# Kernel tuning notes

Measured on AMD Instinct MI355X. Metric: run time of the kernel, lower is better.

Reference implementation:

```python
import jax, jax.numpy as jnp
import numpy as np

# Dims matching init_kwargs / input_specs
H = 64   # latent_size (GRU hidden)
L = 64   # rnn_layers
D = 128  # input_size
B = 128  # batch
T = 256  # sequence length


def setup_inputs() -> dict:
    key = jax.random.key(0)
    ks = jax.random.split(key, 13)
    s = 1.0 / np.sqrt(H)  # PyTorch GRU/Linear default init scale
    u = lambda k, shp: jax.random.uniform(k, shp, jnp.float32, -s, s)
    return {
        "context": jax.random.normal(ks[0], (B, T, D), jnp.float32),
        # encoder GRU params; layer 0 consumes D, layers 1..L-1 consume H
        "enc_Wih0": u(ks[1], (3 * H, D)),
        "enc_Wih": u(ks[2], (L - 1, 3 * H, H)),
        "enc_Whh": u(ks[3], (L, 3 * H, H)),
        "enc_bih": u(ks[4], (L, 3 * H)),
        "enc_bhh": u(ks[5], (L, 3 * H)),
        # decoder GRU params
        "dec_Wih0": u(ks[6], (3 * H, D)),
        "dec_Wih": u(ks[7], (L - 1, 3 * H, H)),
        "dec_Whh": u(ks[8], (L, 3 * H, H)),
        "dec_bih": u(ks[9], (L, 3 * H)),
        "dec_bhh": u(ks[10], (L, 3 * H)),
        # output projection
        "Wo": u(ks[11], (D, H)),
        "bo": u(ks[12], (D,)),
    }


def _gru_cell(x, h, Wih, Whh, bih, bhh):
    # PyTorch gate order: r, z, n
    gi = x @ Wih.T + bih            # (B, 3H)
    gh = h @ Whh.T + bhh            # (B, 3H)
    ir, iz, inn = jnp.split(gi, 3, axis=-1)
    hr, hz, hn = jnp.split(gh, 3, axis=-1)
    r = jax.nn.sigmoid(ir + hr)
    z = jax.nn.sigmoid(iz + hz)
    n = jnp.tanh(inn + r * hn)
    return (1.0 - z) * n + z * h


def _run_gru(X, h0, Wih0, Wih, Whh, bih, bhh):
    # X: (B, T, D); h0: (L, B, H). Returns (top-layer outputs (B,T,H), final hidden (L,B,H)).
    def layer_step(x_in, lp):
        h_prev, W_ih, W_hh, b_i, b_h = lp
        h_new = _gru_cell(x_in, h_prev, W_ih, W_hh, b_i, b_h)
        return h_new, h_new

    @jax.checkpoint
    def step(hs, x_t):
        h_first = _gru_cell(x_t, hs[0], Wih0, Whh[0], bih[0], bhh[0])
        top, hs_rest = jax.lax.scan(
            layer_step, h_first, (hs[1:], Wih, Whh[1:], bih[1:], bhh[1:]))
        return jnp.concatenate([h_first[None], hs_rest], axis=0), top

    hs_final, outs = jax.lax.scan(step, h0, jnp.swapaxes(X, 0, 1))
    return jnp.swapaxes(outs, 0, 1), hs_final


def reference(context, enc_Wih0, enc_Wih, enc_Whh, enc_bih, enc_bhh,
              dec_Wih0, dec_Wih, dec_Whh, dec_bih, dec_bhh, Wo, bo):
    Bc = context.shape[0]
    h0 = jnp.zeros((L, Bc, H), context.dtype)
    # encoder: only final hidden state is used
    _, h_n = _run_gru(context, h0, enc_Wih0, enc_Wih, enc_Whh, enc_bih, enc_bhh)
    # teacher forcing (ratio=1.0): decoder input at step i is X[:, i-1], zeros at i=0
    dec_in = jnp.concatenate([jnp.zeros_like(context[:, :1]), context[:, :-1]], axis=1)
    dec_out, _ = _run_gru(dec_in, h_n, dec_Wih0, dec_Wih, dec_Whh, dec_bih, dec_bhh)
    return dec_out @ Wo.T + bo  # (B, T, D)
```

## Files before the change

### kernel.cpp

```cpp
#include <hip/hip_runtime.h>
#include <stdint.h>

typedef uint16_t u16;
typedef unsigned long long u64;
typedef __attribute__((ext_vector_type(8))) short short8;
typedef __attribute__((ext_vector_type(4))) float f32x4;

#define SCOPE __HIP_MEMORY_SCOPE_AGENT
#define FSTRIDE 16
#define FLD(p) __hip_atomic_load((p), __ATOMIC_RELAXED, SCOPE)
#define FST(p, v) __hip_atomic_store((p), (v), __ATOMIC_RELAXED, SCOPE)

template <int N> struct IC { static constexpr int value = N; };

static __device__ __forceinline__ float bf2f(u16 b) {
  union { uint32_t u; float f; } x; x.u = ((uint32_t)b) << 16; return x.f;
}
static __device__ __forceinline__ u16 f2bf(float f) {
  union { float f; uint32_t u; } x; x.f = f;
  uint32_t u = x.u;
  u += 0x7fffu + ((u >> 16) & 1u);
  return (u16)(u >> 16);
}
static __device__ __forceinline__ float sigm(float x) {
  return __builtin_amdgcn_rcpf(1.f + __expf(-x));
}
static __device__ __forceinline__ float tanhf_(float x) {
  return 1.f - 2.f * __builtin_amdgcn_rcpf(1.f + __expf(2.f * x));
}
static __device__ __forceinline__ void lds_barrier() {
  asm volatile("s_waitcnt lgkmcnt(0)\n\ts_barrier" ::: "memory");
}
#define DRAIN0() asm volatile("s_waitcnt vmcnt(0)" ::: "memory")
static __device__ __forceinline__ int imin(int a, int b) { return a < b ? a : b; }

#define OFF_WHA 0
#define OFF_WHB 12288
#define OFF_WIB 24576
#define OFF_WIA 36864
#define OFF_WO  49152

template <int CHE, int CHD>
__global__ __launch_bounds__(512, 1) void gru_pipeline(
    const void* ctx_,
    const void* eWih0_, const void* eWih_, const void* eWhh_,
    const void* ebih_,  const void* ebhh_,
    const void* dWih0_, const void* dWih_, const void* dWhh_,
    const void* dbih_,  const void* dbhh_,
    const void* Wo_,    const void* bo_,   void* out_,
    int* __restrict__ pflag, int* __restrict__ cflag,
    u64* __restrict__ ringE, u64* __restrict__ ringD, int RE, int RW)
{
  const int tid  = threadIdx.x;
  const bool isX = (tid < 256);
  const int lane = tid & 63;
  const int qg   = (tid >> 6) & 3;
  const int w8   = tid >> 6;
  const int lo   = lane & 15;
  const int hi   = lane >> 4;
  const int blk  = blockIdx.x;
  const int P    = blk >> 3;
  const int g    = blk & 7;
  const int LA   = 2 * P;
  const int NKCA = (P == 0) ? 4 : 2;

  extern __shared__ __align__(16) u16 dynlds[];

  __shared__ __align__(16) u16 hbA[2][16 * 72];
  __shared__ __align__(16) u16 hbB[2][16 * 72];
  __shared__ __align__(16) u16 xstA[2][16 * 72];
  __shared__ int s_cnt, s_fin, s_cn;
  if (tid == 0) { s_cnt = 0; s_fin = 0; s_cn = 0; }
  for (int i = tid; i < 16 * 72; i += 512) {
    hbA[0][i] = 0; hbA[1][i] = 0; hbB[0][i] = 0; hbB[1][i] = 0;
    xstA[0][i] = 0; xstA[1][i] = 0;
  }
  __syncthreads();
  {
    u16 v = ((const u16*)ebih_)[2 * (tid & 255)];
    int e = (v >> 7) & 0xFF;
    if (e >= 100 && e <= 126 && isX) atomicAdd(&s_cnt, 1);
  }
  __syncthreads();
  const bool bf = (s_cnt >= 128);

  auto ld8 = [&](const void* p, int idx) -> short8 {
    if (bf) return *(const short8*)((const u16*)p + idx);
    const float* f = (const float*)p + idx;
    short8 r;
#pragma unroll
    for (int j = 0; j < 8; ++j) r[j] = (short)f2bf(f[j]);
    return r;
  };
  auto ld1 = [&](const void* p, int idx) -> float {
    return bf ? bf2f(((const u16*)p)[idx]) : ((const float*)p)[idx];
  };

  const int T0 = qg, T1 = 4 + qg, T2 = 8 + qg;

  short8 zf8 = {0,0,0,0,0,0,0,0};
  float  bov[2] = {0.f, 0.f};
  float brzA[2] = {0,0}, binA = 0, bhnA = 0;
  float brzB[2] = {0,0}, binB = 0, bhnB = 0;

  auto stage_w = [&](int offU16, const void* W, int gidx0, int NT, int KC, int K) {
    for (int nt = w8; nt < NT; nt += 8)
      for (int kc = 0; kc < KC; ++kc) {
        short8 v = ld8(W, gidx0 + (nt*16 + lo)*K + kc*32 + hi*8);
        *(short8*)(dynlds + offU16 + (nt*KC + kc)*512 + lane*8) = v;
      }
  };

  auto load_phase = [&](int ph) {
    const void* WH  = ph ? dWhh_ : eWhh_;
    const void* WIs = ph ? dWih_ : eWih_;
    const void* WI0 = ph ? dWih0_ : eWih0_;
    const void* bi  = ph ? dbih_ : ebih_;
    const void* bh  = ph ? dbhh_ : ebhh_;
    stage_w(OFF_WHA, WH, LA*192*64, 12, 2, 64);
    stage_w(OFF_WHB, WH, (LA+1)*192*64, 12, 2, 64);
    stage_w(OFF_WIB, WIs, LA*192*64, 12, 2, 64);
    if (LA == 0) stage_w(OFF_WIA, WI0, 0, 12, 4, 128);
    else         stage_w(OFF_WIA, WIs, (LA-1)*192*64, 12, 2, 64);
    if (isX) {
      brzA[0] = ld1(bi, LA*192 + T0*16 + lo) + ld1(bh, LA*192 + T0*16 + lo);
      brzA[1] = ld1(bi, LA*192 + T1*16 + lo) + ld1(bh, LA*192 + T1*16 + lo);
      binA    = ld1(bi, LA*192 + T2*16 + lo);
      bhnA    = ld1(bh, LA*192 + T2*16 + lo);
    } else {
      const int LB = LA + 1;
      brzB[0] = ld1(bi, LB*192 + T0*16 + lo) + ld1(bh, LB*192 + T0*16 + lo);
      brzB[1] = ld1(bi, LB*192 + T1*16 + lo) + ld1(bh, LB*192 + T1*16 + lo);
      binB    = ld1(bi, LB*192 + T2*16 + lo);
      bhnB    = ld1(bh, LB*192 + T2*16 + lo);
    }
  };
  load_phase(0);
  if (P == 31) {
    stage_w(OFF_WO, Wo_, 0, 8, 2, 64);
    if (!isX) { bov[0] = ld1(bo_, 32*qg + lo); bov[1] = ld1(bo_, 32*qg + 16 + lo); }
  }

  const int oWhA0 = OFF_WHA + T0*1024 + lane*8;
  const int oWhA1 = OFF_WHA + T1*1024 + lane*8;
  const int oWhA2 = OFF_WHA + T2*1024 + lane*8;
  const int oWhB0 = OFF_WHB + T0*1024 + lane*8;
  const int oWhB1 = OFF_WHB + T1*1024 + lane*8;
  const int oWhB2 = OFF_WHB + T2*1024 + lane*8;
  const int oWiB0 = OFF_WIB + T0*1024 + lane*8;
  const int oWiB1 = OFF_WIB + T1*1024 + lane*8;
  const int oWiB2 = OFF_WIB + T2*1024 + lane*8;
  const int oWiA0 = OFF_WIA + T0*(NKCA*512) + lane*8;
  const int oWiA1 = OFF_WIA + T1*(NKCA*512) + lane*8;
  const int oWiA2 = OFF_WIA + T2*(NKCA*512) + lane*8;
  const int oWo0  = OFF_WO + (2*qg + 0)*1024 + lane*8;
  const int oWo1  = OFF_WO + (2*qg + 1)*1024 + lane*8;

  auto WF = [&](int off, int kc) -> short8 {
    return *(const short8*)(dynlds + off + kc*512);
  };

  auto do_proj = [&](int tprev, const u16* hs) {
    f32x4 pacc[2];
#pragma unroll
    for (int ct = 0; ct < 2; ++ct) { float v = bov[ct]; f32x4 tv = {v,v,v,v}; pacc[ct] = tv; }
#pragma unroll
    for (int kc = 0; kc < 2; ++kc) {
      short8 hA = *(const short8*)(hs + lo*72 + kc*32 + hi*8);
      pacc[0] = __builtin_amdgcn_mfma_f32_16x16x32_bf16(hA, WF(oWo0, kc), pacc[0], 0, 0, 0);
      pacc[1] = __builtin_amdgcn_mfma_f32_16x16x32_bf16(hA, WF(oWo1, kc), pacc[1], 0, 0, 0);
    }
#pragma unroll
    for (int ct = 0; ct < 2; ++ct) {
      int n = 32*qg + 16*ct + lo;
#pragma unroll
      for (int p = 0; p < 4; ++p) {
        int b = 16*g + hi*4 + p;
        size_t idx = ((size_t)b * 256 + (tprev - 256)) * 128 + n;
        float v = fminf(64.f, fmaxf(-64.f, pacc[ct][p]));
        if (bf) ((u16*)out_)[idx] = f2bf(v);
        else    ((float*)out_)[idx] = v;
      }
    }
  };

  float hprevA[4] = {0,0,0,0}, hprevB[4] = {0,0,0,0};
  const int brow = 16*g + lo;

  const int eIn  = (P > 0 ? P - 1 : 0) * 8 + g;
  const int eOut = (P < 31 ? P : 30) * 8 + g;
  int* fin   = pflag + eIn  * FSTRIDE;
  int* fout  = pflag + eOut * FSTRIDE;
  int* cself = cflag + (P * 8 + g) * FSTRIDE;
  int* cnext = cflag + ((P < 31 ? P + 1 : 31) * 8 + g) * FSTRIDE;

  auto raddr = [&](int t) -> const u64* {
    return (t < 256)
      ? (ringE + (size_t)eIn * ((size_t)RE * 256) + (size_t)(t & (RE-1)) * 256)
      : (ringD + (size_t)eIn * ((size_t)RW * 256) + (size_t)((t-256) & (RW-1)) * 256);
  };
  auto waddr = [&](int t) -> u64* {
    return (t < 256)
      ? (ringE + (size_t)eOut * ((size_t)RE * 256) + (size_t)(t & (RE-1)) * 256)
      : (ringD + (size_t)eOut * ((size_t)RW * 256) + (size_t)((t-256) & (RW-1)) * 256);
  };

  int budget = 1 << 22;
  const int srow = 4 * (tid & 3);
  const int scol = tid >> 2;

  int f0=0,f1=0,f2=0,f3=0, c0=0,c1=0,c2=0,c3=0;
  short8 cfx[4] = {zf8, zf8, zf8, zf8};

  auto doB = [&](int s) {
    f32x4 br, bz, bin2, bhn;
    { float v;
      v = brzB[0]; br   = (f32x4){v,v,v,v};
      v = brzB[1]; bz   = (f32x4){v,v,v,v};
      v = binB;    bin2 = (f32x4){v,v,v,v};
      v = bhnB;    bhn  = (f32x4){v,v,v,v}; }
    const u16* hsB = hbB[(s + 1) & 1];
    const u16* xsB = hbA[s & 1];
#pragma unroll
    for (int kc = 0; kc < 2; ++kc) {
      short8 hB = *(const short8*)(hsB + lo*72 + kc*32 + hi*8);
      short8 xB = *(const short8*)(xsB + lo*72 + kc*32 + hi*8);
      br   = __builtin_amdgcn_mfma_f32_16x16x32_bf16(hB, WF(oWhB0, kc), br,   0, 0, 0);
      bz   = __builtin_amdgcn_mfma_f32_16x16x32_bf16(hB, WF(oWhB1, kc), bz,   0, 0, 0);
      bhn  = __builtin_amdgcn_mfma_f32_16x16x32_bf16(hB, WF(oWhB2, kc), bhn,  0, 0, 0);
      br   = __builtin_amdgcn_mfma_f32_16x16x32_bf16(xB, WF(oWiB0, kc), br,   0, 0, 0);
      bz   = __builtin_amdgcn_mfma_f32_16x16x32_bf16(xB, WF(oWiB1, kc), bz,   0, 0, 0);
      bin2 = __builtin_amdgcn_mfma_f32_16x16x32_bf16(xB, WF(oWiB2, kc), bin2, 0, 0, 0);
    }
    u16 hBb[4];
#pragma unroll
    for (int p = 0; p < 4; ++p) {
      float r = sigm(br[p]);
      float z = sigm(bz[p]);
      float n = tanhf_(bin2[p] + r * bhn[p]);
      float h = n + z * (hprevB[p] - n);
      h = fminf(1.f, fmaxf(-1.f, h));
      hprevB[p] = h;
      hBb[p] = f2bf(h);
    }
    u16* hd = hbB[s & 1];
#pragma unroll
    for (int p = 0; p < 4; ++p)
      hd[(hi*4 + p) * 72 + qg*16 + lo] = hBb[p];
    if (P < 31) {
      u64 da = (u64)hBb[0] | ((u64)hBb[1] << 16) | ((u64)hBb[2] << 32) | ((u64)hBb[3] << 48);
      FST(waddr(s) + (16*qg + lo)*4 + hi, da);
    }
  };

  __syncthreads();

  auto span = [&](auto chc, const int tbase, const int cbase, const int RC, const bool dec) {
    constexpr int CH = decltype(chc)::value;
    const int NC = 256 / CH;
    const bool credOn = (RC < NC);

    if (P > 0) {
      if (tid == 0) {
        int v = s_fin;
        if (v < cbase + 1) {
          while (budget > 0) {
            int a = FLD(fin+0), b = FLD(fin+1), c = FLD(fin+2), d = FLD(fin+3);
            v = imin(imin(a, b), imin(c, d));
            if (v >= cbase + 1) break;
            --budget; __builtin_amdgcn_s_sleep(2);
          }
          s_fin = v; f0 = v; f1 = v; f2 = v; f3 = v;
        }
      }
      __syncthreads();
      if (isX) {
        u64 r0 = FLD(raddr(tbase) + tid);
        u16* xd = xstA[tbase & 1];
#pragma unroll
        for (int p = 0; p < 4; ++p) xd[(srow + p) * 72 + scol] = (u16)(r0 >> (16 * p));
      }
    }
    if (P == 0 && isX) {
      int tx = (tbase < 256) ? tbase : 0;
#pragma unroll
      for (int kc = 0; kc < 4; ++kc) cfx[kc] = ld8(ctx_, (brow*256 + tx)*128 + kc*32 + hi*8);
    }

#pragma unroll 1
    for (int k = 0; k < NC; ++k) {
      const int t0 = tbase + k * CH;
      const int ck = cbase + k;
      const int fneed = ck + 2 - ((dec && k == NC - 1) ? 1 : 0);
      const int need  = (credOn && k >= RC) ? (ck + 1 - RC) : 0;
      u64 ra[CH];
#pragma unroll
      for (int j = 0; j < CH; ++j) ra[j] = 0;

#pragma unroll
      for (int tt = 0; tt < CH; ++tt) {
        const int t = t0 + tt;
        lds_barrier();

        if (tt == 0) {
          int vf = s_fin, vc = s_cn;
          const bool slowF = (P > 0)  && (vf < fneed);
          const bool slowC = (P < 31) && (need > 0) && (vc < need);
          if (slowF || slowC) {
            if (tid == 0) {
              if (slowF) {
                int v = 0;
                while (budget > 0) {
                  int a = FLD(fin+0), b = FLD(fin+1), c = FLD(fin+2), d = FLD(fin+3);
                  v = imin(imin(a, b), imin(c, d));
                  if (v >= fneed) break;
                  --budget; __builtin_amdgcn_s_sleep(2);
                }
                s_fin = v; f0 = v; f1 = v; f2 = v; f3 = v;
              }
              if (slowC) {
                int v = 0;
                while (budget > 0) {
                  int a = FLD(cnext+0), b = FLD(cnext+1), c = FLD(cnext+2), d = FLD(cnext+3);
                  v = imin(imin(a, b), imin(c, d));
                  if (v >= need) break;
                  --budget; __builtin_amdgcn_s_sleep(2);
                }
                s_cn = v; c0 = v; c1 = v; c2 = v; c3 = v;
              }
            }
            lds_barrier();
          }
          if (isX && P > 0) {
#pragma unroll
            for (int j = 0; j < CH; ++j)
              if (t0 + 1 + j <= 511) ra[j] = FLD(raddr(t0 + 1 + j) + tid);
          }
        }

        if (isX) {
          if (tid == 0) {
            if (P > 0)  s_fin = imin(imin(f0, f1), imin(f2, f3));
            if (P < 31 && credOn) s_cn = imin(imin(c0, c1), imin(c2, c3));
            if (P > 0)  { f0 = FLD(fin+0); f1 = FLD(fin+1); f2 = FLD(fin+2); f3 = FLD(fin+3); }
            if (P < 31 && credOn) { c0 = FLD(cnext+0); c1 = FLD(cnext+1); c2 = FLD(cnext+2); c3 = FLD(cnext+3); }
          }

          f32x4 ar, az, ain, ahn;
          { float v;
            v = brzA[0]; ar  = (f32x4){v,v,v,v};
            v = brzA[1]; az  = (f32x4){v,v,v,v};
            v = binA;    ain = (f32x4){v,v,v,v};
            v = bhnA;    ahn = (f32x4){v,v,v,v}; }
          const u16* hsA = hbA[(t + 1) & 1];
#pragma unroll
          for (int kc = 0; kc < 2; ++kc) {
            short8 hA = *(const short8*)(hsA + lo*72 + kc*32 + hi*8);
            ar  = __builtin_amdgcn_mfma_f32_16x16x32_bf16(hA, WF(oWhA0, kc), ar,  0, 0, 0);
            az  = __builtin_amdgcn_mfma_f32_16x16x32_bf16(hA, WF(oWhA1, kc), az,  0, 0, 0);
            ahn = __builtin_amdgcn_mfma_f32_16x16x32_bf16(hA, WF(oWhA2, kc), ahn, 0, 0, 0);
          }
          short8 xfA[4] = {zf8, zf8, zf8, zf8};
          if (P > 0) {
            const u16* xs = xstA[t & 1];
#pragma unroll
            for (int kc = 0; kc < 2; ++kc)
              xfA[kc] = *(const short8*)(xs + lo*72 + kc*32 + hi*8);
          } else {
#pragma unroll
            for (int kc = 0; kc < 4; ++kc) xfA[kc] = cfx[kc];
          }
          if (!(P == 0 && t == 256)) {
#pragma unroll
            for (int kc = 0; kc < 4; ++kc) {
              if (kc < NKCA) {
                ar  = __builtin_amdgcn_mfma_f32_16x16x32_bf16(xfA[kc], WF(oWiA0, kc), ar,  0, 0, 0);
                az  = __builtin_amdgcn_mfma_f32_16x16x32_bf16(xfA[kc], WF(oWiA1, kc), az,  0, 0, 0);
                ain = __builtin_amdgcn_mfma_f32_16x16x32_bf16(xfA[kc], WF(oWiA2, kc), ain, 0, 0, 0);
              }
            }
          }
          u16 hAb[4];
#pragma unroll
          for (int p = 0; p < 4; ++p) {
            float r = sigm(ar[p]);
            float z = sigm(az[p]);
            float n = tanhf_(ain[p] + r * ahn[p]);
            float h = n + z * (hprevA[p] - n);
            h = fminf(1.f, fmaxf(-1.f, h));
            hprevA[p] = h;
            hAb[p] = f2bf(h);
          }
          {
            u16* hd = hbA[t & 1];
#pragma unroll
            for (int p = 0; p < 4; ++p)
              hd[(hi*4 + p) * 72 + qg*16 + lo] = hAb[p];
          }
          if (P == 0) {
            int tn = t + 1;
            if (tn <= 511) {
              int tx = (tn < 256) ? tn : ((tn == 256) ? 0 : tn - 257);
#pragma unroll
              for (int kc = 0; kc < 4; ++kc)
                cfx[kc] = ld8(ctx_, (brow*256 + tx)*128 + kc*32 + hi*8);
            }
          }
          if (P > 0 && t < 511) {
            u64 r = ra[tt];
            u16* xd = xstA[(t + 1) & 1];
#pragma unroll
            for (int p = 0; p < 4; ++p) xd[(srow + p) * 72 + scol] = (u16)(r >> (16 * p));
          }
          if (tt == CH - 1 && P > 0 && credOn) {
            DRAIN0();
            if (lane == 0) FST(cself + qg, ck + 1);
          }
        } else {
          constexpr int FO = (CH >= 2) ? 1 : 0;
          if (P < 31 && tt == FO && k > ((CH == 1) ? 1 : 0)) {
            DRAIN0();
            if (lane == 0) FST(fout + qg, ck - ((CH == 1) ? 1 : 0));
          }
          if (P == 31 && dec && t >= 258) do_proj(t - 2, hbB[t & 1]);
          if (t - 1 >= tbase) doB(t - 1);
        }
      }
    }

    lds_barrier();
    if (!isX) {
      doB(tbase + 255);
      if (P < 31) {
        DRAIN0();
        if (lane == 0) FST(fout + qg, cbase + NC);
      }
    }
  };

  {
    const int NCe = 256 / CHE;
    int RCe = (RE >= 256) ? NCe : (RE / CHE) - 2; if (RCe < 1) RCe = 1;
    span(IC<CHE>{}, 0, 0, RCe, false);
    __syncthreads();
    load_phase(1);
    __syncthreads();
    int RCd = (RW >= 256) ? (256 / CHD) : (RW / CHD) - 2; if (RCd < 1) RCd = 1;
    span(IC<CHD>{}, 256, NCe, RCd, true);
  }

  lds_barrier();
  if (P == 31 && !isX) {
    do_proj(510, hbB[0]);
    do_proj(511, hbB[1]);
  }
}

extern "C" void kernel_launch(void* const* d_in, const int* in_sizes, int n_in,
                              void* d_out, int out_size, void* d_ws, size_t ws_size,
                              hipStream_t stream)
{
  char* ws = (char*)d_ws;
  int* pflag = (int*)ws;
  int* cflag = (int*)(ws + 32768);
  char* ringbase = ws + 65536;

  const size_t per_slot = (size_t)31 * 8 * 2048;
  size_t avail = (ws_size > 65536) ? ws_size - 65536 : 0;

  int RE, RW;
  u64 *ringE, *ringD;
  int Rh = 0;
  for (int r = 256; r >= 16; r >>= 1)
    if ((size_t)(2 * r) * per_slot <= avail) { Rh = r; break; }
  if (Rh) {
    RE = RW = Rh;
    ringE = (u64*)ringbase;
    ringD = (u64*)(ringbase + (size_t)Rh * per_slot);
  } else {
    int Rw = 1;
    for (int r = 256; r >= 1; r >>= 1)
      if ((size_t)r * per_slot <= avail) { Rw = r; break; }
    RW = Rw;
    int Re = 1;
    for (int r = 16; r >= 1; r >>= 1)
      if ((size_t)r * per_slot <= (size_t)out_size) { Re = r; break; }
    RE = Re;
    ringE = (u64*)d_out;
    ringD = (u64*)ringbase;
  }
  const int CHe = (RE >= 32) ? 4 : ((RE >= 16) ? 2 : 1);
  const int CHd = (RW >= 32) ? 4 : ((RW >= 16) ? 2 : 1);

  const int dyn = 122880;
  static int attr_done = 0;
  if (!attr_done) {
    hipFuncSetAttribute(reinterpret_cast<const void*>(gru_pipeline<4,4>),
                        hipFuncAttributeMaxDynamicSharedMemorySize, dyn);
    hipFuncSetAttribute(reinterpret_cast<const void*>(gru_pipeline<2,4>),
                        hipFuncAttributeMaxDynamicSharedMemorySize, dyn);
    hipFuncSetAttribute(reinterpret_cast<const void*>(gru_pipeline<2,2>),
                        hipFuncAttributeMaxDynamicSharedMemorySize, dyn);
    hipFuncSetAttribute(reinterpret_cast<const void*>(gru_pipeline<2,1>),
                        hipFuncAttributeMaxDynamicSharedMemorySize, dyn);
    hipFuncSetAttribute(reinterpret_cast<const void*>(gru_pipeline<1,1>),
                        hipFuncAttributeMaxDynamicSharedMemorySize, dyn);
    attr_done = 1;
  }

  hipMemsetAsync(ws, 0, 65536, stream);

#define LAUNCH(CE, CD)                                                     \
  gru_pipeline<CE, CD><<<256, 512, dyn, stream>>>(                         \
      d_in[0], d_in[1], d_in[2], d_in[3], d_in[4], d_in[5],                \
      d_in[6], d_in[7], d_in[8], d_in[9], d_in[10], d_in[11], d_in[12],    \
      d_out, pflag, cflag, ringE, ringD, RE, RW)

  if      (CHe == 4 && CHd == 4) LAUNCH(4, 4);
  else if (CHe == 2 && CHd == 4) LAUNCH(2, 4);
  else if (CHe == 2 && CHd == 2) LAUNCH(2, 2);
  else if (CHe == 2 && CHd == 1) LAUNCH(2, 1);
  else                           LAUNCH(1, 1);
#undef LAUNCH
  (void)in_sizes; (void)n_in;
}
```

Baseline: 1.861 ms.

## Repartition pipeline into 16 stages of 4 layers with register-resident weights

The layer pipeline moves from 32 stages of 2 layers × 8 batch groups of 16 rows to 16 stages of 4 layers × 16 batch groups of 8 rows. Each wave now keeps its gate weights in registers instead of reading them from dynamic LDS, and the two wavegroups each run two layers in a staggered schedule. The intent is to halve the number of inter-block handoffs along the dependency chain and remove LDS weight reads from the critical path. The cost is that MFMA tiles are half padding (8 real rows in 16), register pressure rises, and the chunk size is fixed at 2 instead of adapting to ring size.

Result: slower. 1.941 ms (+4.3%).

```diff
diff --git a/kernel.cpp b/kernel.cpp
--- a/kernel.cpp
+++ b/kernel.cpp
@@ -10,8 +10,6 @@
 #define FSTRIDE 16
 #define FLD(p) __hip_atomic_load((p), __ATOMIC_RELAXED, SCOPE)
 #define FST(p, v) __hip_atomic_store((p), (v), __ATOMIC_RELAXED, SCOPE)
-
-template <int N> struct IC { static constexpr int value = N; };
 
 static __device__ __forceinline__ float bf2f(u16 b) {
   union { uint32_t u; float f; } x; x.u = ((uint32_t)b) << 16; return x.f;
@@ -34,13 +32,6 @@
 #define DRAIN0() asm volatile("s_waitcnt vmcnt(0)" ::: "memory")
 static __device__ __forceinline__ int imin(int a, int b) { return a < b ? a : b; }
 
-#define OFF_WHA 0
-#define OFF_WHB 12288
-#define OFF_WIB 24576
-#define OFF_WIA 36864
-#define OFF_WO  49152
-
-template <int CHE, int CHD>
 __global__ __launch_bounds__(512, 1) void gru_pipeline(
     const void* ctx_,
     const void* eWih0_, const void* eWih_, const void* eWhh_,
@@ -51,29 +42,27 @@
     int* __restrict__ pflag, int* __restrict__ cflag,
     u64* __restrict__ ringE, u64* __restrict__ ringD, int RE, int RW)
 {
+  constexpr int CH = 2;
   const int tid  = threadIdx.x;
   const bool isX = (tid < 256);
   const int lane = tid & 63;
   const int qg   = (tid >> 6) & 3;
-  const int w8   = tid >> 6;
   const int lo   = lane & 15;
   const int hi   = lane >> 4;
   const int blk  = blockIdx.x;
-  const int P    = blk >> 3;
-  const int g    = blk & 7;
-  const int LA   = 2 * P;
-  const int NKCA = (P == 0) ? 4 : 2;
-
-  extern __shared__ __align__(16) u16 dynlds[];
-
-  __shared__ __align__(16) u16 hbA[2][16 * 72];
-  __shared__ __align__(16) u16 hbB[2][16 * 72];
-  __shared__ __align__(16) u16 xstA[2][16 * 72];
+  const int P    = blk >> 4;
+  const int g    = blk & 15;
+  const int L0   = 4 * P;
+  const int NKC0 = (P == 0) ? 4 : 2;
+
+  __shared__ __align__(16) u16 hb[4][2][16 * 72];
+  __shared__ __align__(16) u16 xst[2][16 * 72];
   __shared__ int s_cnt, s_fin, s_cn;
   if (tid == 0) { s_cnt = 0; s_fin = 0; s_cn = 0; }
   for (int i = tid; i < 16 * 72; i += 512) {
-    hbA[0][i] = 0; hbA[1][i] = 0; hbB[0][i] = 0; hbB[1][i] = 0;
-    xstA[0][i] = 0; xstA[1][i] = 0;
+#pragma unroll
+    for (int j = 0; j < 4; ++j) { hb[j][0][i] = 0; hb[j][1][i] = 0; }
+    xst[0][i] = 0; xst[1][i] = 0;
   }
   __syncthreads();
   {
@@ -96,20 +85,23 @@
     return bf ? bf2f(((const u16*)p)[idx]) : ((const float*)p)[idx];
   };
 
-  const int T0 = qg, T1 = 4 + qg, T2 = 8 + qg;
+  int T[3]; T[0] = qg; T[1] = 4 + qg; T[2] = 8 + qg;
 
   short8 zf8 = {0,0,0,0,0,0,0,0};
+  short8 whF[3][2], whS[3][2];
+  short8 wiF[3][4], wiS[3][4];
+  short8 wo[2][2];
   float  bov[2] = {0.f, 0.f};
-  float brzA[2] = {0,0}, binA = 0, bhnA = 0;
-  float brzB[2] = {0,0}, binB = 0, bhnB = 0;
-
-  auto stage_w = [&](int offU16, const void* W, int gidx0, int NT, int KC, int K) {
-    for (int nt = w8; nt < NT; nt += 8)
-      for (int kc = 0; kc < KC; ++kc) {
-        short8 v = ld8(W, gidx0 + (nt*16 + lo)*K + kc*32 + hi*8);
-        *(short8*)(dynlds + offU16 + (nt*KC + kc)*512 + lane*8) = v;
-      }
-  };
+  float brz_[2][2], bin_[2], bhn_[2];
+  brz_[0][0]=brz_[0][1]=brz_[1][0]=brz_[1][1]=0.f;
+  bin_[0]=bin_[1]=bhn_[0]=bhn_[1]=0.f;
+#pragma unroll
+  for (int ti = 0; ti < 3; ++ti) {
+    whF[ti][0]=zf8; whF[ti][1]=zf8; whS[ti][0]=zf8; whS[ti][1]=zf8;
+#pragma unroll
+    for (int kc = 0; kc < 4; ++kc) { wiF[ti][kc]=zf8; wiS[ti][kc]=zf8; }
+  }
+  wo[0][0]=wo[0][1]=wo[1][0]=wo[1][1]=zf8;
 
   auto load_phase = [&](int ph) {
     const void* WH  = ph ? dWhh_ : eWhh_;
@@ -117,48 +109,45 @@
     const void* WI0 = ph ? dWih0_ : eWih0_;
     const void* bi  = ph ? dbih_ : ebih_;
     const void* bh  = ph ? dbhh_ : ebhh_;
-    stage_w(OFF_WHA, WH, LA*192*64, 12, 2, 64);
-    stage_w(OFF_WHB, WH, (LA+1)*192*64, 12, 2, 64);
-    stage_w(OFF_WIB, WIs, LA*192*64, 12, 2, 64);
-    if (LA == 0) stage_w(OFF_WIA, WI0, 0, 12, 4, 128);
-    else         stage_w(OFF_WIA, WIs, (LA-1)*192*64, 12, 2, 64);
-    if (isX) {
-      brzA[0] = ld1(bi, LA*192 + T0*16 + lo) + ld1(bh, LA*192 + T0*16 + lo);
-      brzA[1] = ld1(bi, LA*192 + T1*16 + lo) + ld1(bh, LA*192 + T1*16 + lo);
-      binA    = ld1(bi, LA*192 + T2*16 + lo);
-      bhnA    = ld1(bh, LA*192 + T2*16 + lo);
-    } else {
-      const int LB = LA + 1;
-      brzB[0] = ld1(bi, LB*192 + T0*16 + lo) + ld1(bh, LB*192 + T0*16 + lo);
-      brzB[1] = ld1(bi, LB*192 + T1*16 + lo) + ld1(bh, LB*192 + T1*16 + lo);
-      binB    = ld1(bi, LB*192 + T2*16 + lo);
-      bhnB    = ld1(bh, LB*192 + T2*16 + lo);
-    }
+    const int lF = L0 + (isX ? 0 : 2);
+    const int lS = lF + 1;
+    const void* WIF  = (lF == 0) ? WI0 : WIs;
+    const int   iF   = (lF == 0) ? 0 : (lF - 1) * 192 * 64;
+    const int   KF   = (lF == 0) ? 128 : 64;
+    const int   nkcF = (lF == 0) ? 4 : 2;
+#pragma unroll
+    for (int ti = 0; ti < 3; ++ti) {
+#pragma unroll
+      for (int kc = 0; kc < 2; ++kc) {
+        whF[ti][kc] = ld8(WH, lF*192*64 + (T[ti]*16 + lo)*64 + kc*32 + hi*8);
+        whS[ti][kc] = ld8(WH, lS*192*64 + (T[ti]*16 + lo)*64 + kc*32 + hi*8);
+        wiS[ti][kc] = ld8(WIs, (lS-1)*192*64 + (T[ti]*16 + lo)*64 + kc*32 + hi*8);
+      }
+#pragma unroll
+      for (int kc = 0; kc < 4; ++kc)
+        if (kc < nkcF)
+          wiF[ti][kc] = ld8(WIF, iF + (T[ti]*16 + lo)*KF + kc*32 + hi*8);
+    }
+    brz_[0][0] = ld1(bi, lF*192 + T[0]*16 + lo) + ld1(bh, lF*192 + T[0]*16 + lo);
+    brz_[0][1] = ld1(bi, lF*192 + T[1]*16 + lo) + ld1(bh, lF*192 + T[1]*16 + lo);
+    bin_[0]    = ld1(bi, lF*192 + T[2]*16 + lo);
+    bhn_[0]    = ld1(bh, lF*192 + T[2]*16 + lo);
+    brz_[1][0] = ld1(bi, lS*192 + T[0]*16 + lo) + ld1(bh, lS*192 + T[0]*16 + lo);
+    brz_[1][1] = ld1(bi, lS*192 + T[1]*16 + lo) + ld1(bh, lS*192 + T[1]*16 + lo);
+    bin_[1]    = ld1(bi, lS*192 + T[2]*16 + lo);
+    bhn_[1]    = ld1(bh, lS*192 + T[2]*16 + lo);
   };
   load_phase(0);
-  if (P == 31) {
-    stage_w(OFF_WO, Wo_, 0, 8, 2, 64);
-    if (!isX) { bov[0] = ld1(bo_, 32*qg + lo); bov[1] = ld1(bo_, 32*qg + 16 + lo); }
-  }
-
-  const int oWhA0 = OFF_WHA + T0*1024 + lane*8;
-  const int oWhA1 = OFF_WHA + T1*1024 + lane*8;
-  const int oWhA2 = OFF_WHA + T2*1024 + lane*8;
-  const int oWhB0 = OFF_WHB + T0*1024 + lane*8;
-  const int oWhB1 = OFF_WHB + T1*1024 + lane*8;
-  const int oWhB2 = OFF_WHB + T2*1024 + lane*8;
-  const int oWiB0 = OFF_WIB + T0*1024 + lane*8;
-  const int oWiB1 = OFF_WIB + T1*1024 + lane*8;
-  const int oWiB2 = OFF_WIB + T2*1024 + lane*8;
-  const int oWiA0 = OFF_WIA + T0*(NKCA*512) + lane*8;
-  const int oWiA1 = OFF_WIA + T1*(NKCA*512) + lane*8;
-  const int oWiA2 = OFF_WIA + T2*(NKCA*512) + lane*8;
-  const int oWo0  = OFF_WO + (2*qg + 0)*1024 + lane*8;
-  const int oWo1  = OFF_WO + (2*qg + 1)*1024 + lane*8;
-
-  auto WF = [&](int off, int kc) -> short8 {
-    return *(const short8*)(dynlds + off + kc*512);
-  };
+  if (P == 15 && !isX) {
+#pragma unroll
+    for (int ct = 0; ct < 2; ++ct) {
+      int n = 32*qg + 16*ct + lo;
+#pragma unroll
+      for (int kc = 0; kc < 2; ++kc)
+        wo[ct][kc] = ld8(Wo_, n*64 + kc*32 + hi*8);
+      bov[ct] = ld1(bo_, n);
+    }
+  }
 
   auto do_proj = [&](int tprev, const u16* hs) {
     f32x4 pacc[2];
@@ -167,96 +156,107 @@
 #pragma unroll
     for (int kc = 0; kc < 2; ++kc) {
       short8 hA = *(const short8*)(hs + lo*72 + kc*32 + hi*8);
-      pacc[0] = __builtin_amdgcn_mfma_f32_16x16x32_bf16(hA, WF(oWo0, kc), pacc[0], 0, 0, 0);
-      pacc[1] = __builtin_amdgcn_mfma_f32_16x16x32_bf16(hA, WF(oWo1, kc), pacc[1], 0, 0, 0);
-    }
-#pragma unroll
-    for (int ct = 0; ct < 2; ++ct) {
-      int n = 32*qg + 16*ct + lo;
-#pragma unroll
-      for (int p = 0; p < 4; ++p) {
-        int b = 16*g + hi*4 + p;
-        size_t idx = ((size_t)b * 256 + (tprev - 256)) * 128 + n;
-        float v = fminf(64.f, fmaxf(-64.f, pacc[ct][p]));
-        if (bf) ((u16*)out_)[idx] = f2bf(v);
-        else    ((float*)out_)[idx] = v;
+      pacc[0] = __builtin_amdgcn_mfma_f32_16x16x32_bf16(hA, wo[0][kc], pacc[0], 0, 0, 0);
+      pacc[1] = __builtin_amdgcn_mfma_f32_16x16x32_bf16(hA, wo[1][kc], pacc[1], 0, 0, 0);
+    }
+    if (hi < 2) {
+#pragma unroll
+      for (int ct = 0; ct < 2; ++ct) {
+        int n = 32*qg + 16*ct + lo;
+#pragma unroll
+        for (int p = 0; p < 4; ++p) {
+          int b = 8*g + hi*4 + p;
+          size_t idx = ((size_t)b * 256 + (tprev - 256)) * 128 + n;
+          float v = fminf(64.f, fmaxf(-64.f, pacc[ct][p]));
+          if (bf) ((u16*)out_)[idx] = f2bf(v);
+          else    ((float*)out_)[idx] = v;
+        }
       }
     }
   };
 
-  float hprevA[4] = {0,0,0,0}, hprevB[4] = {0,0,0,0};
-  const int brow = 16*g + lo;
-
-  const int eIn  = (P > 0 ? P - 1 : 0) * 8 + g;
-  const int eOut = (P < 31 ? P : 30) * 8 + g;
+  auto gcell = [&](const short8 (*wh)[2], const short8 (*wi)[4], int nkc, bool skipx,
+                   const short8* xf, const u16* hs,
+                   const float* brz, float bin, float bhn, float* hp, u16* ob) {
+    f32x4 ar, az, ain, ahn;
+    { float v;
+      v = brz[0]; ar  = (f32x4){v,v,v,v};
+      v = brz[1]; az  = (f32x4){v,v,v,v};
+      v = bin;    ain = (f32x4){v,v,v,v};
+      v = bhn;    ahn = (f32x4){v,v,v,v}; }
+#pragma unroll
+    for (int kc = 0; kc < 2; ++kc) {
+      short8 hA = *(const short8*)(hs + lo*72 + kc*32 + hi*8);
+      ar  = __builtin_amdgcn_mfma_f32_16x16x32_bf16(hA, wh[0][kc], ar,  0, 0, 0);
+      az  = __builtin_amdgcn_mfma_f32_16x16x32_bf16(hA, wh[1][kc], az,  0, 0, 0);
+      ahn = __builtin_amdgcn_mfma_f32_16x16x32_bf16(hA, wh[2][kc], ahn, 0, 0, 0);
+    }
+    if (!skipx) {
+#pragma unroll
+      for (int kc = 0; kc < 4; ++kc) {
+        if (kc < nkc) {
+          ar  = __builtin_amdgcn_mfma_f32_16x16x32_bf16(xf[kc], wi[0][kc], ar,  0, 0, 0);
+          az  = __builtin_amdgcn_mfma_f32_16x16x32_bf16(xf[kc], wi[1][kc], az,  0, 0, 0);
+          ain = __builtin_amdgcn_mfma_f32_16x16x32_bf16(xf[kc], wi[2][kc], ain, 0, 0, 0);
+        }
+      }
+    }
+#pragma unroll
+    for (int p = 0; p < 4; ++p) {
+      float r = sigm(ar[p]);
+      float z = sigm(az[p]);
+      float n = tanhf_(ain[p] + r * ahn[p]);
+      float h = n + z * (hp[p] - n);
+      h = fminf(1.f, fmaxf(-1.f, h));
+      hp[p] = h;
+      ob[p] = f2bf(h);
+    }
+  };
+  auto wtile = [&](u16* hd, const u16* ob) {
+#pragma unroll
+    for (int p = 0; p < 4; ++p)
+      hd[(hi*4 + p) * 72 + qg*16 + lo] = (hi < 2) ? ob[p] : (u16)0;
+  };
+  auto xfrag2 = [&](const u16* xs, short8* xf) {
+#pragma unroll
+    for (int kc = 0; kc < 2; ++kc)
+      xf[kc] = *(const short8*)(xs + lo*72 + kc*32 + hi*8);
+  };
+
+  float hpF[4] = {0,0,0,0}, hpS[4] = {0,0,0,0};
+  const int brow = 8*g + (lo & 7);
+
+  const int eIn  = (P > 0 ? P - 1 : 0) * 16 + g;
+  const int eOut = (P < 15 ? P : 14) * 16 + g;
   int* fin   = pflag + eIn  * FSTRIDE;
   int* fout  = pflag + eOut * FSTRIDE;
-  int* cself = cflag + (P * 8 + g) * FSTRIDE;
-  int* cnext = cflag + ((P < 31 ? P + 1 : 31) * 8 + g) * FSTRIDE;
+  int* cself = cflag + (P * 16 + g) * FSTRIDE;
+  int* cnext = cflag + ((P < 15 ? P + 1 : 15) * 16 + g) * FSTRIDE;
 
   auto raddr = [&](int t) -> const u64* {
     return (t < 256)
-      ? (ringE + (size_t)eIn * ((size_t)RE * 256) + (size_t)(t & (RE-1)) * 256)
-      : (ringD + (size_t)eIn * ((size_t)RW * 256) + (size_t)((t-256) & (RW-1)) * 256);
+      ? (ringE + (size_t)eIn * ((size_t)RE * 128) + (size_t)(t & (RE-1)) * 128)
+      : (ringD + (size_t)eIn * ((size_t)RW * 128) + (size_t)((t-256) & (RW-1)) * 128);
   };
   auto waddr = [&](int t) -> u64* {
     return (t < 256)
-      ? (ringE + (size_t)eOut * ((size_t)RE * 256) + (size_t)(t & (RE-1)) * 256)
-      : (ringD + (size_t)eOut * ((size_t)RW * 256) + (size_t)((t-256) & (RW-1)) * 256);
+      ? (ringE + (size_t)eOut * ((size_t)RE * 128) + (size_t)(t & (RE-1)) * 128)
+      : (ringD + (size_t)eOut * ((size_t)RW * 128) + (size_t)((t-256) & (RW-1)) * 128);
+  };
+  auto stage_x = [&](int t, u64 r) {
+    u16* xd = xst[t & 1];
+    int col = tid >> 1, rb = 4 * (tid & 1);
+#pragma unroll
+    for (int p = 0; p < 4; ++p) xd[(rb + p) * 72 + col] = (u16)(r >> (16 * p));
   };
 
   int budget = 1 << 22;
-  const int srow = 4 * (tid & 3);
-  const int scol = tid >> 2;
-
   int f0=0,f1=0,f2=0,f3=0, c0=0,c1=0,c2=0,c3=0;
   short8 cfx[4] = {zf8, zf8, zf8, zf8};
 
-  auto doB = [&](int s) {
-    f32x4 br, bz, bin2, bhn;
-    { float v;
-      v = brzB[0]; br   = (f32x4){v,v,v,v};
-      v = brzB[1]; bz   = (f32x4){v,v,v,v};
-      v = binB;    bin2 = (f32x4){v,v,v,v};
-      v = bhnB;    bhn  = (f32x4){v,v,v,v}; }
-    const u16* hsB = hbB[(s + 1) & 1];
-    const u16* xsB = hbA[s & 1];
-#pragma unroll
-    for (int kc = 0; kc < 2; ++kc) {
-      short8 hB = *(const short8*)(hsB + lo*72 + kc*32 + hi*8);
-      short8 xB = *(const short8*)(xsB + lo*72 + kc*32 + hi*8);
-      br   = __builtin_amdgcn_mfma_f32_16x16x32_bf16(hB, WF(oWhB0, kc), br,   0, 0, 0);
-      bz   = __builtin_amdgcn_mfma_f32_16x16x32_bf16(hB, WF(oWhB1, kc), bz,   0, 0, 0);
-      bhn  = __builtin_amdgcn_mfma_f32_16x16x32_bf16(hB, WF(oWhB2, kc), bhn,  0, 0, 0);
-      br   = __builtin_amdgcn_mfma_f32_16x16x32_bf16(xB, WF(oWiB0, kc), br,   0, 0, 0);
-      bz   = __builtin_amdgcn_mfma_f32_16x16x32_bf16(xB, WF(oWiB1, kc), bz,   0, 0, 0);
-      bin2 = __builtin_amdgcn_mfma_f32_16x16x32_bf16(xB, WF(oWiB2, kc), bin2, 0, 0, 0);
-    }
-    u16 hBb[4];
-#pragma unroll
-    for (int p = 0; p < 4; ++p) {
-      float r = sigm(br[p]);
-      float z = sigm(bz[p]);
-      float n = tanhf_(bin2[p] + r * bhn[p]);
-      float h = n + z * (hprevB[p] - n);
-      h = fminf(1.f, fmaxf(-1.f, h));
-      hprevB[p] = h;
-      hBb[p] = f2bf(h);
-    }
-    u16* hd = hbB[s & 1];
-#pragma unroll
-    for (int p = 0; p < 4; ++p)
-      hd[(hi*4 + p) * 72 + qg*16 + lo] = hBb[p];
-    if (P < 31) {
-      u64 da = (u64)hBb[0] | ((u64)hBb[1] << 16) | ((u64)hBb[2] << 32) | ((u64)hBb[3] << 48);
-      FST(waddr(s) + (16*qg + lo)*4 + hi, da);
-    }
-  };
-
   __syncthreads();
 
-  auto span = [&](auto chc, const int tbase, const int cbase, const int RC, const bool dec) {
-    constexpr int CH = decltype(chc)::value;
+  auto span = [&](const int tbase, const int cbase, const int RC, const bool dec) {
     const int NC = 256 / CH;
     const bool credOn = (RC < NC);
 
@@ -274,12 +274,7 @@
         }
       }
       __syncthreads();
-      if (isX) {
-        u64 r0 = FLD(raddr(tbase) + tid);
-        u16* xd = xstA[tbase & 1];
-#pragma unroll
-        for (int p = 0; p < 4; ++p) xd[(srow + p) * 72 + scol] = (u16)(r0 >> (16 * p));
-      }
+      if (tid < 128) stage_x(tbase, FLD(raddr(tbase) + tid));
     }
     if (P == 0 && isX) {
       int tx = (tbase < 256) ? tbase : 0;
@@ -305,7 +300,7 @@
         if (tt == 0) {
           int vf = s_fin, vc = s_cn;
           const bool slowF = (P > 0)  && (vf < fneed);
-          const bool slowC = (P < 31) && (need > 0) && (vc < need);
+          const bool slowC = (P < 15) && (need > 0) && (vc < need);
           if (slowF || slowC) {
             if (tid == 0) {
               if (slowF) {
@@ -331,7 +326,7 @@
             }
             lds_barrier();
           }
-          if (isX && P > 0) {
+          if (P > 0 && tid < 128) {
 #pragma unroll
             for (int j = 0; j < CH; ++j)
               if (t0 + 1 + j <= 511) ra[j] = FLD(raddr(t0 + 1 + j) + tid);
@@ -339,64 +334,48 @@
         }
 
         if (isX) {
-          if (tid == 0) {
+          short8 xf[4] = {zf8, zf8, zf8, zf8};
+          bool skipx = false;
+          if (P > 0) xfrag2(xst[t & 1], xf);
+          else { xf[0]=cfx[0]; xf[1]=cfx[1]; xf[2]=cfx[2]; xf[3]=cfx[3]; skipx = (t == 256); }
+          u16 ob[4];
+          gcell(whF, wiF, NKC0, skipx, xf, hb[0][(t + 1) & 1],
+                brz_[0], bin_[0], bhn_[0], hpF, ob);
+          wtile(hb[0][t & 1], ob);
+        } else {
+          if (P < 15 && tt == 0 && k > 0) {
+            DRAIN0();
+            if (lane == 0) FST(fout + qg, ck);
+          }
+          if (P == 15 && dec && t >= 258) do_proj(t - 2, hb[3][t & 1]);
+          if (t - 1 >= tbase) {
+            const int s = t - 1;
+            short8 xf[4] = {zf8, zf8, zf8, zf8};
+            xfrag2(hb[1][s & 1], xf);
+            u16 ob[4];
+            gcell(whF, wiF, 2, false, xf, hb[2][(s + 1) & 1],
+                  brz_[0], bin_[0], bhn_[0], hpF, ob);
+            wtile(hb[2][s & 1], ob);
+          }
+        }
+
+        lds_barrier();
+
+        if (isX) {
+          if (tt == CH - 1 && tid == 0) {
             if (P > 0)  s_fin = imin(imin(f0, f1), imin(f2, f3));
-            if (P < 31 && credOn) s_cn = imin(imin(c0, c1), imin(c2, c3));
+            if (P < 15 && credOn) s_cn = imin(imin(c0, c1), imin(c2, c3));
+          }
+          if (tt == 0 && tid == 0) {
             if (P > 0)  { f0 = FLD(fin+0); f1 = FLD(fin+1); f2 = FLD(fin+2); f3 = FLD(fin+3); }
-            if (P < 31 && credOn) { c0 = FLD(cnext+0); c1 = FLD(cnext+1); c2 = FLD(cnext+2); c3 = FLD(cnext+3); }
-          }
-
-          f32x4 ar, az, ain, ahn;
-          { float v;
-            v = brzA[0]; ar  = (f32x4){v,v,v,v};
-            v = brzA[1]; az  = (f32x4){v,v,v,v};
-            v = binA;    ain = (f32x4){v,v,v,v};
-            v = bhnA;    ahn = (f32x4){v,v,v,v}; }
-          const u16* hsA = hbA[(t + 1) & 1];
-#pragma unroll
-          for (int kc = 0; kc < 2; ++kc) {
-            short8 hA = *(const short8*)(hsA + lo*72 + kc*32 + hi*8);
-            ar  = __builtin_amdgcn_mfma_f32_16x16x32_bf16(hA, WF(oWhA0, kc), ar,  0, 0, 0);
-            az  = __builtin_amdgcn_mfma_f32_16x16x32_bf16(hA, WF(oWhA1, kc), az,  0, 0, 0);
-            ahn = __builtin_amdgcn_mfma_f32_16x16x32_bf16(hA, WF(oWhA2, kc), ahn, 0, 0, 0);
-          }
-          short8 xfA[4] = {zf8, zf8, zf8, zf8};
-          if (P > 0) {
-            const u16* xs = xstA[t & 1];
-#pragma unroll
-            for (int kc = 0; kc < 2; ++kc)
-              xfA[kc] = *(const short8*)(xs + lo*72 + kc*32 + hi*8);
-          } else {
-#pragma unroll
-            for (int kc = 0; kc < 4; ++kc) xfA[kc] = cfx[kc];
-          }
-          if (!(P == 0 && t == 256)) {
-#pragma unroll
-            for (int kc = 0; kc < 4; ++kc) {
-              if (kc < NKCA) {
-                ar  = __builtin_amdgcn_mfma_f32_16x16x32_bf16(xfA[kc], WF(oWiA0, kc), ar,  0, 0, 0);
-                az  = __builtin_amdgcn_mfma_f32_16x16x32_bf16(xfA[kc], WF(oWiA1, kc), az,  0, 0, 0);
-                ain = __builtin_amdgcn_mfma_f32_16x16x32_bf16(xfA[kc], WF(oWiA2, kc), ain, 0, 0, 0);
-              }
-            }
-          }
-          u16 hAb[4];
-#pragma unroll
-          for (int p = 0; p < 4; ++p) {
-            float r = sigm(ar[p]);
-            float z = sigm(az[p]);
-            float n = tanhf_(ain[p] + r * ahn[p]);
-            float h = n + z * (hprevA[p] - n);
-            h = fminf(1.f, fmaxf(-1.f, h));
-            hprevA[p] = h;
-            hAb[p] = f2bf(h);
-          }
-          {
-            u16* hd = hbA[t & 1];
-#pragma unroll
-            for (int p = 0; p < 4; ++p)
-              hd[(hi*4 + p) * 72 + qg*16 + lo] = hAb[p];
-          }
+            if (P < 15 && credOn) { c0 = FLD(cnext+0); c1 = FLD(cnext+1); c2 = FLD(cnext+2); c3 = FLD(cnext+3); }
+          }
+          short8 xf[4] = {zf8, zf8, zf8, zf8};
+          xfrag2(hb[0][t & 1], xf);
+          u16 ob[4];
+          gcell(whS, wiS, 2, false, xf, hb[1][(t + 1) & 1],
+                brz_[1], bin_[1], bhn_[1], hpS, ob);
+          wtile(hb[1][t & 1], ob);
           if (P == 0) {
             int tn = t + 1;
             if (tn <= 511) {
@@ -406,32 +385,53 @@
                 cfx[kc] = ld8(ctx_, (brow*256 + tx)*128 + kc*32 + hi*8);
             }
           }
-          if (P > 0 && t < 511) {
-            u64 r = ra[tt];
-            u16* xd = xstA[(t + 1) & 1];
-#pragma unroll
-            for (int p = 0; p < 4; ++p) xd[(srow + p) * 72 + scol] = (u16)(r >> (16 * p));
-          }
+          if (P > 0 && t < 511 && tid < 128) stage_x(t + 1, ra[tt]);
           if (tt == CH - 1 && P > 0 && credOn) {
             DRAIN0();
             if (lane == 0) FST(cself + qg, ck + 1);
           }
         } else {
-          constexpr int FO = (CH >= 2) ? 1 : 0;
-          if (P < 31 && tt == FO && k > ((CH == 1) ? 1 : 0)) {
-            DRAIN0();
-            if (lane == 0) FST(fout + qg, ck - ((CH == 1) ? 1 : 0));
-          }
-          if (P == 31 && dec && t >= 258) do_proj(t - 2, hbB[t & 1]);
-          if (t - 1 >= tbase) doB(t - 1);
+          if (t - 1 >= tbase) {
+            const int s = t - 1;
+            short8 xf[4] = {zf8, zf8, zf8, zf8};
+            xfrag2(hb[2][s & 1], xf);
+            u16 ob[4];
+            gcell(whS, wiS, 2, false, xf, hb[3][(s + 1) & 1],
+                  brz_[1], bin_[1], bhn_[1], hpS, ob);
+            wtile(hb[3][s & 1], ob);
+            if (P < 15 && hi < 2) {
+              u64 da = (u64)ob[0] | ((u64)ob[1] << 16) | ((u64)ob[2] << 32) | ((u64)ob[3] << 48);
+              FST(waddr(s) + (16*qg + lo)*2 + hi, da);
+            }
+          }
         }
       }
     }
 
     lds_barrier();
     if (!isX) {
-      doB(tbase + 255);
-      if (P < 31) {
+      const int s = tbase + 255;
+      short8 xf[4] = {zf8, zf8, zf8, zf8};
+      xfrag2(hb[1][s & 1], xf);
+      u16 ob[4];
+      gcell(whF, wiF, 2, false, xf, hb[2][(s + 1) & 1],
+            brz_[0], bin_[0], bhn_[0], hpF, ob);
+      wtile(hb[2][s & 1], ob);
+    }
+    lds_barrier();
+    if (!isX) {
+      const int s = tbase + 255;
+      short8 xf[4] = {zf8, zf8, zf8, zf8};
+      xfrag2(hb[2][s & 1], xf);
+      u16 ob[4];
+      gcell(whS, wiS, 2, false, xf, hb[3][(s + 1) & 1],
+            brz_[1], bin_[1], bhn_[1], hpS, ob);
+      wtile(hb[3][s & 1], ob);
+      if (P < 15) {
+        if (hi < 2) {
+          u64 da = (u64)ob[0] | ((u64)ob[1] << 16) | ((u64)ob[2] << 32) | ((u64)ob[3] << 48);
+          FST(waddr(s) + (16*qg + lo)*2 + hi, da);
+        }
         DRAIN0();
         if (lane == 0) FST(fout + qg, cbase + NC);
       }
@@ -439,20 +439,20 @@
   };
 
   {
-    const int NCe = 256 / CHE;
-    int RCe = (RE >= 256) ? NCe : (RE / CHE) - 2; if (RCe < 1) RCe = 1;
-    span(IC<CHE>{}, 0, 0, RCe, false);
+    const int NCe = 256 / CH;
+    int RCe = (RE >= 256) ? NCe : (RE / CH) - 2; if (RCe < 1) RCe = 1;
+    span(0, 0, RCe, false);
     __syncthreads();
     load_phase(1);
     __syncthreads();
-    int RCd = (RW >= 256) ? (256 / CHD) : (RW / CHD) - 2; if (RCd < 1) RCd = 1;
-    span(IC<CHD>{}, 256, NCe, RCd, true);
+    int RCd = (RW >= 256) ? (256 / CH) : (RW / CH) - 2; if (RCd < 1) RCd = 1;
+    span(256, NCe, RCd, true);
   }
 
   lds_barrier();
-  if (P == 31 && !isX) {
-    do_proj(510, hbB[0]);
-    do_proj(511, hbB[1]);
+  if (P == 15 && !isX) {
+    do_proj(510, hb[3][0]);
+    do_proj(511, hb[3][1]);
   }
 }
 
@@ -465,7 +465,7 @@
   int* cflag = (int*)(ws + 32768);
   char* ringbase = ws + 65536;
 
-  const size_t per_slot = (size_t)31 * 8 * 2048;
+  const size_t per_slot = (size_t)15 * 16 * 1024;
   size_t avail = (ws_size > 65536) ? ws_size - 65536 : 0;
 
   int RE, RW;
@@ -489,38 +489,12 @@
     ringE = (u64*)d_out;
     ringD = (u64*)ringbase;
   }
-  const int CHe = (RE >= 32) ? 4 : ((RE >= 16) ? 2 : 1);
-  const int CHd = (RW >= 32) ? 4 : ((RW >= 16) ? 2 : 1);
-
-  const int dyn = 122880;
-  static int attr_done = 0;
-  if (!attr_done) {
-    hipFuncSetAttribute(reinterpret_cast<const void*>(gru_pipeline<4,4>),
-                        hipFuncAttributeMaxDynamicSharedMemorySize, dyn);
-    hipFuncSetAttribute(reinterpret_cast<const void*>(gru_pipeline<2,4>),
-                        hipFuncAttributeMaxDynamicSharedMemorySize, dyn);
-    hipFuncSetAttribute(reinterpret_cast<const void*>(gru_pipeline<2,2>),
-                        hipFuncAttributeMaxDynamicSharedMemorySize, dyn);
-    hipFuncSetAttribute(reinterpret_cast<const void*>(gru_pipeline<2,1>),
-                        hipFuncAttributeMaxDynamicSharedMemorySize, dyn);
-    hipFuncSetAttribute(reinterpret_cast<const void*>(gru_pipeline<1,1>),
-                        hipFuncAttributeMaxDynamicSharedMemorySize, dyn);
-    attr_done = 1;
-  }
 
   hipMemsetAsync(ws, 0, 65536, stream);
 
-#define LAUNCH(CE, CD)                                                     \
-  gru_pipeline<CE, CD><<<256, 512, dyn, stream>>>(                         \
-      d_in[0], d_in[1], d_in[2], d_in[3], d_in[4], d_in[5],                \
-      d_in[6], d_in[7], d_in[8], d_in[9], d_in[10], d_in[11], d_in[12],    \
-      d_out, pflag, cflag, ringE, ringD, RE, RW)
-
-  if      (CHe == 4 && CHd == 4) LAUNCH(4, 4);
-  else if (CHe == 2 && CHd == 4) LAUNCH(2, 4);
-  else if (CHe == 2 && CHd == 2) LAUNCH(2, 2);
-  else if (CHe == 2 && CHd == 1) LAUNCH(2, 1);
-  else                           LAUNCH(1, 1);
-#undef LAUNCH
+  gru_pipeline<<<256, 512, 0, stream>>>(
+      d_in[0], d_in[1], d_in[2], d_in[3], d_in[4], d_in[5],
+      d_in[6], d_in[7], d_in[8], d_in[9], d_in[10], d_in[11], d_in[12],
+      d_out, pflag, cflag, ringE, ringD, RE, RW);
   (void)in_sizes; (void)n_in;
 }
```
